# Kernel tuning notes

Measured on AMD Instinct MI355X. Metric: run time of the kernel, lower is better.

## Reference

```python
import jax, jax.numpy as jnp
import numpy as np

B, H, W, C = 32, 56, 56, 256
K = 7  # spatial-attention conv kernel size


def setup_inputs() -> dict:
    key = jax.random.key(0)
    kx, kw = jax.random.split(key)
    x = jax.random.normal(kx, (B, H, W, C), dtype=jnp.float32)
    # he_normal init for a 7x7 conv with 2 input channels
    fan_in = K * K * 2
    conv_w = jax.random.normal(kw, (K, K, 2, 1), dtype=jnp.float32) * jnp.sqrt(2.0 / fan_in)
    return {"x": x, "conv_w": conv_w}


def reference(x, conv_w):
    # channel-wise avg and max pooling -> [B,H,W,2]
    avg_pool = jnp.mean(x, axis=-1, keepdims=True)
    max_pool = jnp.max(x, axis=-1, keepdims=True)
    concat = jnp.concatenate([avg_pool, max_pool], axis=-1)
    # 7x7 conv, 2 -> 1 channels, SAME padding, no bias, sigmoid activation
    attn = jax.lax.conv_general_dilated(
        concat, conv_w,
        window_strides=(1, 1), padding="SAME",
        dimension_numbers=("NHWC", "HWIO", "NHWC"),
    )
    attn = jax.nn.sigmoid(attn)  # [B,H,W,1]
    return x * attn
```

## Files before the change

### kernel.cpp

```cpp
#include <hip/hip_runtime.h>
#include <math.h>

#define BB 32
#define HH 56
#define WW 56
#define CC 256
#define KS 7
#define NPIX (BB * HH * WW)

typedef float vfloat4 __attribute__((ext_vector_type(4)));

__global__ __launch_bounds__(256) void pool_kernel(const float* __restrict__ x,
                                                   float2* __restrict__ pooled) {
    const int wave = threadIdx.x >> 6;
    const int lane = threadIdx.x & 63;
    const int pix = blockIdx.x * 4 + wave;

    const vfloat4 v = reinterpret_cast<const vfloat4*>(x)[(size_t)pix * (CC / 4) + lane];
    float s = v.x + v.y + v.z + v.w;
    float m = fmaxf(fmaxf(v.x, v.y), fmaxf(v.z, v.w));

#pragma unroll
    for (int off = 32; off > 0; off >>= 1) {
        s += __shfl_down(s, off, 64);
        m = fmaxf(m, __shfl_down(m, off, 64));
    }
    if (lane == 0) {
        pooled[pix] = make_float2(s * (1.0f / CC), m);
    }
}

__global__ __launch_bounds__(256) void fused_kernel(const float* __restrict__ x,
                                                    const float2* __restrict__ pooled,
                                                    const float2* __restrict__ cwv,
                                                    float* __restrict__ out) {
    const int wave = threadIdx.x >> 6;
    const int lane = threadIdx.x & 63;
    const int pix = blockIdx.x * 4 + wave;

    const size_t i = (size_t)pix * (CC / 4) + lane;
    const vfloat4 v = reinterpret_cast<const vfloat4*>(x)[i];

    const int wcol = pix % WW;
    const int t = pix / WW;
    const int hrow = t % HH;
    const int b = t / HH;

    float partial = 0.0f;
    if (lane < KS * KS) {
        const int ky = lane / KS;
        const int kx = lane - ky * KS;
        const int yy = hrow + ky - 3;
        const int xx = wcol + kx - 3;
        if (yy >= 0 && yy < HH && xx >= 0 && xx < WW) {
            const float2 p = pooled[((size_t)b * HH + yy) * WW + xx];
            const float2 w = cwv[lane];
            partial = fmaf(p.x, w.x, p.y * w.y);
        }
    }
#pragma unroll
    for (int off = 1; off < 64; off <<= 1) {
        partial += __shfl_xor(partial, off, 64);
    }
    const float att = 1.0f / (1.0f + expf(-partial));

    vfloat4 o = v * att;
    reinterpret_cast<vfloat4*>(out)[i] = o;
}

extern "C" void kernel_launch(void* const* d_in, const int* in_sizes, int n_in,
                              void* d_out, int out_size, void* d_ws, size_t ws_size,
                              hipStream_t stream) {
    const float* x = (const float*)d_in[0];
    const float* cw = (const float*)d_in[1];
    float* out = (float*)d_out;

    float2* pooled = (float2*)d_ws;

    pool_kernel<<<NPIX / 4, 256, 0, stream>>>(x, pooled);

    fused_kernel<<<NPIX / 4, 256, 0, stream>>>(x, pooled, (const float2*)cw, out);
}
```

Before: 54.72 us.

## Process two pixels per wave and use DPP wave reductions

Each wave now handles two adjacent pixels in both the pooling and the fused multiply kernels, which halves the grid and amortises index math, the weight load and reduction overhead. Shuffle-based reductions are replaced with DPP row operations followed by a readlane. The second pixel shares the same row and reuses the loaded weights. The trade-offs are fewer waves in flight, more registers per thread, and extra reduction work per wave.

```diff
diff --git a/kernel.cpp b/kernel.cpp
--- a/kernel.cpp
+++ b/kernel.cpp
@@ -7,26 +7,64 @@
 #define CC 256
 #define KS 7
 #define NPIX (BB * HH * WW)
+#define NWPAIR (NPIX / 2)
 
 typedef float vfloat4 __attribute__((ext_vector_type(4)));
 
+template <int CTRL, int RM, int BM>
+__device__ __forceinline__ float dpp_add(float v) {
+    const int iv = __float_as_int(v);
+    const int sh = __builtin_amdgcn_update_dpp(iv, iv, CTRL, RM, BM, false);
+    return v + __int_as_float(sh);
+}
+template <int CTRL, int RM, int BM>
+__device__ __forceinline__ float dpp_max(float v) {
+    const int iv = __float_as_int(v);
+    const int sh = __builtin_amdgcn_update_dpp(iv, iv, CTRL, RM, BM, false);
+    return fmaxf(v, __int_as_float(sh));
+}
+
+__device__ __forceinline__ float wave_sum(float s) {
+    s = dpp_add<0x111, 0xf, 0xf>(s);
+    s = dpp_add<0x112, 0xf, 0xf>(s);
+    s = dpp_add<0x114, 0xf, 0xe>(s);
+    s = dpp_add<0x118, 0xf, 0xc>(s);
+    s = dpp_add<0x142, 0xa, 0xf>(s);
+    s = dpp_add<0x143, 0xc, 0xf>(s);
+    return __int_as_float(__builtin_amdgcn_readlane(__float_as_int(s), 63));
+}
+__device__ __forceinline__ float wave_max(float m) {
+    m = dpp_max<0x111, 0xf, 0xf>(m);
+    m = dpp_max<0x112, 0xf, 0xf>(m);
+    m = dpp_max<0x114, 0xf, 0xe>(m);
+    m = dpp_max<0x118, 0xf, 0xc>(m);
+    m = dpp_max<0x142, 0xa, 0xf>(m);
+    m = dpp_max<0x143, 0xc, 0xf>(m);
+    return __int_as_float(__builtin_amdgcn_readlane(__float_as_int(m), 63));
+}
+
 __global__ __launch_bounds__(256) void pool_kernel(const float* __restrict__ x,
-                                                   float2* __restrict__ pooled) {
+                                                   float4* __restrict__ pooled4) {
     const int wave = threadIdx.x >> 6;
     const int lane = threadIdx.x & 63;
-    const int pix = blockIdx.x * 4 + wave;
+    const int wid = blockIdx.x * 4 + wave;
 
-    const vfloat4 v = reinterpret_cast<const vfloat4*>(x)[(size_t)pix * (CC / 4) + lane];
-    float s = v.x + v.y + v.z + v.w;
-    float m = fmaxf(fmaxf(v.x, v.y), fmaxf(v.z, v.w));
+    const size_t base = (size_t)wid * 128 + lane;
+    const vfloat4 v0 = reinterpret_cast<const vfloat4*>(x)[base];
+    const vfloat4 v1 = reinterpret_cast<const vfloat4*>(x)[base + 64];
 
-#pragma unroll
-    for (int off = 32; off > 0; off >>= 1) {
-        s += __shfl_down(s, off, 64);
-        m = fmaxf(m, __shfl_down(m, off, 64));
-    }
+    float s0 = (v0.x + v0.y) + (v0.z + v0.w);
+    float m0 = fmaxf(fmaxf(v0.x, v0.y), fmaxf(v0.z, v0.w));
+    float s1 = (v1.x + v1.y) + (v1.z + v1.w);
+    float m1 = fmaxf(fmaxf(v1.x, v1.y), fmaxf(v1.z, v1.w));
+
+    s0 = wave_sum(s0);
+    s1 = wave_sum(s1);
+    m0 = wave_max(m0);
+    m1 = wave_max(m1);
+
     if (lane == 0) {
-        pooled[pix] = make_float2(s * (1.0f / CC), m);
+        pooled4[wid] = make_float4(s0 * (1.0f / CC), m0, s1 * (1.0f / CC), m1);
     }
 }
 
@@ -36,48 +74,56 @@
                                                     float* __restrict__ out) {
     const int wave = threadIdx.x >> 6;
     const int lane = threadIdx.x & 63;
-    const int pix = blockIdx.x * 4 + wave;
+    const int wid = blockIdx.x * 4 + wave;
 
-    const size_t i = (size_t)pix * (CC / 4) + lane;
-    const vfloat4 v = reinterpret_cast<const vfloat4*>(x)[i];
+    const size_t base = (size_t)wid * 128 + lane;
+    const vfloat4 v0 = reinterpret_cast<const vfloat4*>(x)[base];
+    const vfloat4 v1 = reinterpret_cast<const vfloat4*>(x)[base + 64];
 
-    const int wcol = pix % WW;
-    const int t = pix / WW;
+    const int pix0 = wid * 2;
+    const int wcol0 = pix0 % WW;
+    const int t = pix0 / WW;
     const int hrow = t % HH;
     const int b = t / HH;
 
-    float partial = 0.0f;
+    float pa = 0.0f, pb = 0.0f;
     if (lane < KS * KS) {
         const int ky = lane / KS;
         const int kx = lane - ky * KS;
         const int yy = hrow + ky - 3;
-        const int xx = wcol + kx - 3;
-        if (yy >= 0 && yy < HH && xx >= 0 && xx < WW) {
-            const float2 p = pooled[((size_t)b * HH + yy) * WW + xx];
+        if (yy >= 0 && yy < HH) {
+            const float2* __restrict__ row = pooled + ((size_t)b * HH + yy) * WW;
             const float2 w = cwv[lane];
-            partial = fmaf(p.x, w.x, p.y * w.y);
+            const int xx0 = wcol0 + kx - 3;
+            const int xx1 = xx0 + 1;
+            if (xx0 >= 0 && xx0 < WW) {
+                const float2 p = row[xx0];
+                pa = fmaf(p.x, w.x, p.y * w.y);
+            }
+            if (xx1 >= 0 && xx1 < WW) {
+                const float2 p = row[xx1];
+                pb = fmaf(p.x, w.x, p.y * w.y);
+            }
         }
     }
-#pragma unroll
-    for (int off = 1; off < 64; off <<= 1) {
-        partial += __shfl_xor(partial, off, 64);
-    }
-    const float att = 1.0f / (1.0f + expf(-partial));
+    pa = wave_sum(pa);
+    pb = wave_sum(pb);
+    const float att0 = 1.0f / (1.0f + expf(-pa));
+    const float att1 = 1.0f / (1.0f + expf(-pb));
 
-    vfloat4 o = v * att;
-    reinterpret_cast<vfloat4*>(out)[i] = o;
+    reinterpret_cast<vfloat4*>(out)[base]      = v0 * att0;
+    reinterpret_cast<vfloat4*>(out)[base + 64] = v1 * att1;
 }
 
 extern "C" void kernel_launch(void* const* d_in, const int* in_sizes, int n_in,
                               void* d_out, int out_size, void* d_ws, size_t ws_size,
                               hipStream_t stream) {
     const float* x = (const float*)d_in[0];
-    const float* cw = (const float*)d_in[1];
+    const float2* cw = (const float2*)d_in[1];
     float* out = (float*)d_out;
-
     float2* pooled = (float2*)d_ws;
 
-    pool_kernel<<<NPIX / 4, 256, 0, stream>>>(x, pooled);
-
-    fused_kernel<<<NPIX / 4, 256, 0, stream>>>(x, pooled, (const float2*)cw, out);
+    const int grid = NWPAIR / 4;
+    pool_kernel<<<grid, 256, 0, stream>>>(x, (float4*)pooled);
+    fused_kernel<<<grid, 256, 0, stream>>>(x, pooled, cw, out);
 }
```

Result: faster. 51.26 us (-6.3%).
